# Optimization experiments

Measured on AMD Instinct MI355X. Metric: run time of the kernel, lower is better.

Reference implementation:

```python
import jax, jax.numpy as jnp
import numpy as np

B, T, F2, F1 = 64, 300, 2944, 1472
RED, H, K, LN = 256, 32, 15, 7          # reduced_size, hidden_size, att_frams, layer_num
CA_RED = 320
N_CROP = T - 2 * (K - 1)                # 272 frames after the two k=15 convs
PYR = [2 ** j for j in range(1, LN)]    # [2,4,8,16,32,64]


def _pool_matrix(N, sizes):
    """Stacked AdaptiveAvgPool1d matrices: rows average torch-style bins."""
    mats = []
    for m in sizes:
        P = np.zeros((m, N), np.float32)
        for i in range(m):
            s = (i * N) // m
            e = -((-(i + 1) * N) // m)  # ceil((i+1)*N/m)
            P[i, s:e] = 1.0 / (e - s)
        mats.append(P)
    return jnp.asarray(np.concatenate(mats, 0))  # [sum(sizes), N]


def setup_inputs() -> dict:
    key = jax.random.key(0)
    ks = jax.random.split(key, 24)
    g = lambda k, sh, s=0.05: (jax.random.normal(k, sh) * s).astype(jnp.float32)
    inp = {
        "input": jax.random.normal(ks[0], (B, T, F2), jnp.float32),
        "input_length": jnp.full((B,), T, jnp.int64),
        "mean_var": g(ks[1], (F1,), 1.0),
        "std_var": jax.random.uniform(ks[2], (F1,), jnp.float32, 0.5, 1.5),
        "mean_mean": g(ks[3], (F1,), 1.0),
        "std_mean": jax.random.uniform(ks[4], (F1,), jnp.float32, 0.5, 1.5),
        # ChannelAttention params
        "ca_fc1_w": g(ks[5], (CA_RED, F2)), "ca_fc1_b": g(ks[6], (CA_RED,)),
        "ca_fc2_w": g(ks[7], (F2, CA_RED)), "ca_fc2_b": g(ks[8], (F2,)),
        # ANN (n_ANNlayers=1 -> only fc0 used)
        "ann_w": g(ks[9], (RED, F1)), "ann_b": g(ks[10], (RED,)),
        # GRU (torch gate order r,z,n)
        "gru_w_ih": g(ks[11], (3 * H, RED)), "gru_w_hh": g(ks[12], (3 * H, H)),
        "gru_b_ih": g(ks[13], (3 * H,)), "gru_b_hh": g(ks[14], (3 * H,)),
        # frame-quality head
        "q_w": g(ks[15], (1, H)), "q_b": g(ks[16], (1,)),
        # temporal attention convs
        "att_w1": g(ks[17], (1, H, K)), "att_b1": g(ks[18], (1,)),
        "att_w2": g(ks[19], (1, 1, K)), "att_b2": g(ks[20], (1,)),
        "qreg2_w": g(ks[21], (1, 2 ** LN - 1)), "qreg2_b": g(ks[22], (1,)),
    }
    return inp


def _gru(x, w_ih, w_hh, b_ih, b_hh):
    xg = jnp.einsum("btf,gf->btg", x, w_ih) + b_ih  # [B,T,3H]

    def step(h, xt):
        hg = h @ w_hh.T + b_hh
        xr, xz, xn = jnp.split(xt, 3, -1)
        hr, hz, hn = jnp.split(hg, 3, -1)
        r = jax.nn.sigmoid(xr + hr)
        z = jax.nn.sigmoid(xz + hz)
        n = jnp.tanh(xn + r * hn)
        h = (1.0 - z) * n + z * h
        return h, h

    h0 = jnp.zeros((x.shape[0], H), x.dtype)
    _, hs = jax.lax.scan(step, h0, jnp.swapaxes(xg, 0, 1))
    return jnp.swapaxes(hs, 0, 1)  # [B,T,H]


def reference(input, input_length, mean_var, std_var, mean_mean, std_mean,
              ca_fc1_w, ca_fc1_b, ca_fc2_w, ca_fc2_b, ann_w, ann_b,
              gru_w_ih, gru_w_hh, gru_b_ih, gru_b_hh, q_w, q_b,
              att_w1, att_b1, att_w2, att_b2, qreg2_w, qreg2_b):
    # --- ChannelAttention: normalize var/mean halves, sigmoid gate, fuse to 1472-d
    x_var = (input[..., :F1] - mean_var) / std_var
    x_mean = (input[..., F1:] - mean_mean) / std_mean
    xn = jnp.concatenate([x_var, x_mean], -1)                      # [B,T,2944]
    w = jax.nn.sigmoid(jnp.maximum(xn @ ca_fc1_w.T + ca_fc1_b, 0.0) @ ca_fc2_w.T + ca_fc2_b)
    feat = w[..., :F1] * x_var + w[..., F1:] * x_mean              # [B,T,1472]

    # --- ANN (single layer) + GRU
    feat = feat @ ann_w.T + ann_b                                  # [B,T,256]
    outs = _gru(feat, gru_w_ih, gru_w_hh, gru_b_ih, gru_b_hh)      # [B,T,32]

    # --- temporal attention: Conv1d(H,1,15) -> ReLU -> Conv1d(1,1,15) -> tanh
    xc = jnp.swapaxes(outs, 1, 2)                                  # [B,H,T]
    dn = ("NCH", "OIH", "NCH")
    a = jax.lax.conv_general_dilated(xc, att_w1, (1,), "VALID", dimension_numbers=dn) + att_b1[None, :, None]
    a = jnp.maximum(a, 0.0)
    a = jax.lax.conv_general_dilated(a, att_w2, (1,), "VALID", dimension_numbers=dn) + att_b2[None, :, None]
    att = jnp.tanh(a[:, 0, :])                                     # [B,N_CROP]

    q_fet = att[..., None] * outs[:, K - 1: T - (K - 1), :]        # [B,N_CROP,H]

    # --- pyramid pooling: row0 = plain mean, rest = attention-weighted means
    P = _pool_matrix(N_CROP, PYR)                                  # [126, N_CROP]
    row0 = q_fet.mean(1, keepdims=True)                            # [B,1,H]
    num = jnp.einsum("mn,bnh->bmh", P, q_fet)                      # [B,126,H]
    den = jnp.einsum("mn,bn->bm", P, att)[..., None]               # [B,126,1]
    q_pool = jnp.concatenate([row0, num / den], 1)                 # [B,127,H]

    q_each = (q_pool @ q_w.T + q_b)[..., 0]                        # [B,127]
    score = q_each @ qreg2_w.T + qreg2_b                           # [B,1]
    return score
```

## Files before the change

kernel.cpp:

```cpp
#include <hip/hip_runtime.h>


typedef unsigned short u16t;
typedef unsigned int   u32t;
typedef float  f32x4 __attribute__((ext_vector_type(4)));
typedef u32t   u32x4 __attribute__((ext_vector_type(4)));
typedef __bf16 bf16x8 __attribute__((ext_vector_type(8)));

__device__ __forceinline__ f32x4 mfma_b(u32x4 a, u32x4 b, f32x4 c){
  return __builtin_amdgcn_mfma_f32_16x16x32_bf16(
      __builtin_bit_cast(bf16x8, a), __builtin_bit_cast(bf16x8, b), c, 0, 0, 0);
}

#define GLDS16(SRC, DST)                                                    \
  __builtin_amdgcn_global_load_lds(                                         \
      (const __attribute__((address_space(1))) void*)(SRC),                 \
      (__attribute__((address_space(3))) void*)(DST), 16, 0, 0)

__device__ __forceinline__ u32t resid(u32t u){
  float d = __uint_as_float(u) - __uint_as_float(u & 0xFFFF0000u);
  return __float_as_uint(d);
}

__device__ __forceinline__ void split8_3(u32x4 a, u32x4 b,
                                         u32x4& H, u32x4& M, u32x4& L){
  u32t r1[8], r2[8];
#pragma unroll
  for (int j = 0; j < 4; j++){ r1[j] = resid(a[j]); r1[4 + j] = resid(b[j]); }
#pragma unroll
  for (int j = 0; j < 8; j++){ r2[j] = resid(r1[j]); }
  H[0] = __builtin_amdgcn_perm(a[1], a[0], 0x07060302u);
  H[1] = __builtin_amdgcn_perm(a[3], a[2], 0x07060302u);
  H[2] = __builtin_amdgcn_perm(b[1], b[0], 0x07060302u);
  H[3] = __builtin_amdgcn_perm(b[3], b[2], 0x07060302u);
  M[0] = __builtin_amdgcn_perm(r1[1], r1[0], 0x07060302u);
  M[1] = __builtin_amdgcn_perm(r1[3], r1[2], 0x07060302u);
  M[2] = __builtin_amdgcn_perm(r1[5], r1[4], 0x07060302u);
  M[3] = __builtin_amdgcn_perm(r1[7], r1[6], 0x07060302u);
  L[0] = __builtin_amdgcn_perm(r2[1], r2[0], 0x07060302u);
  L[1] = __builtin_amdgcn_perm(r2[3], r2[2], 0x07060302u);
  L[2] = __builtin_amdgcn_perm(r2[5], r2[4], 0x07060302u);
  L[3] = __builtin_amdgcn_perm(r2[7], r2[6], 0x07060302u);
}

__device__ __forceinline__ void mfma6(const u32x4& AH, const u32x4& AM, const u32x4& AL,
                                      const u32x4& BH, const u32x4& BM, const u32x4& BL,
                                      f32x4& acc){
  acc = mfma_b(AL, BH, acc);
  acc = mfma_b(AM, BM, acc);
  acc = mfma_b(AH, BL, acc);
  acc = mfma_b(AM, BH, acc);
  acc = mfma_b(AH, BM, acc);
  acc = mfma_b(AH, BH, acc);
}

__global__ __launch_bounds__(256) void prep_params_kernel(
    const float* __restrict__ mv, const float* __restrict__ sv,
    const float* __restrict__ mm, const float* __restrict__ sm,
    double* __restrict__ mu, double* __restrict__ rinv){
  int f = blockIdx.x * 256 + threadIdx.x;
  if (f < 2944){
    if (f < 1472){ mu[f] = (double)mv[f]; rinv[f] = 1.0 / (double)sv[f]; }
    else         { mu[f] = (double)mm[f - 1472]; rinv[f] = 1.0 / (double)sm[f - 1472]; }
  }
}

__global__ __launch_bounds__(256) void fold_w1_kernel(
    const float* __restrict__ w, const double* __restrict__ rinv,
    float* __restrict__ w1p){
  int id = blockIdx.x * 256 + threadIdx.x;
  if (id < 320 * 2944)
    w1p[id] = (float)((double)w[id] * rinv[id % 2944]);
}

__global__ __launch_bounds__(64) void b1p_kernel(
    const float* __restrict__ w1, const float* __restrict__ b1,
    const double* __restrict__ mu, const double* __restrict__ rinv,
    float* __restrict__ b1p){
  int n = blockIdx.x, lane = threadIdx.x;
  double s = 0.0;
  for (int k = lane; k < 2944; k += 64)
    s += (double)w1[n * 2944 + k] * rinv[k] * mu[k];
#pragma unroll
  for (int o = 32; o > 0; o >>= 1) s += __shfl_xor(s, o);
  if (lane == 0) b1p[n] = (float)((double)b1[n] - s);
}

__global__ __launch_bounds__(256) void make_wc_kernel(
    const float* __restrict__ wih, const float* __restrict__ annw,
    const float* __restrict__ annb, const float* __restrict__ bih,
    float* __restrict__ wc, float* __restrict__ bc){
  int id = blockIdx.x * 256 + threadIdx.x;
  if (id < 96 * 1472){
    int g = id / 1472, k = id - g * 1472;
    double s = 0.0;
    for (int r = 0; r < 256; r++)
      s += (double)wih[g * 256 + r] * (double)annw[r * 1472 + k];
    wc[id] = (float)s;
  } else if (id < 96 * 1472 + 96){
    int g = id - 96 * 1472;
    double s = (double)bih[g];
    for (int r = 0; r < 256; r++)
      s += (double)wih[g * 256 + r] * (double)annb[r];
    bc[g] = (float)s;
  }
}

__global__ __launch_bounds__(256) void gemm1_kernel(
    const float* __restrict__ x, const float* __restrict__ w1p,
    const float* __restrict__ b1p, float* __restrict__ h1){
  __shared__ float lA[80 * 32];
  __shared__ float lB[320 * 32];
  const int tid = threadIdx.x, wave = tid >> 6, lane = tid & 63;
  const int m0 = blockIdx.x * 80;
  const int l8 = lane >> 3, l7 = lane & 7;
  f32x4 acc[5][5] = {};
  for (int k0 = 0; k0 < 2944; k0 += 32){
    __syncthreads();
    for (int i = wave; i < 10; i += 4){
      int row = i * 8 + l8;
      GLDS16(x + (size_t)(m0 + row) * 2944 + k0 + ((l7 ^ (row & 7)) << 2), lA + (i << 8));
    }
    for (int i = wave; i < 40; i += 4){
      int row = i * 8 + l8;
      GLDS16(w1p + (size_t)row * 2944 + k0 + ((l7 ^ (row & 7)) << 2), lB + (i << 8));
    }
    __syncthreads();
    const int g = lane >> 4, r15 = lane & 15;
    u32x4 AH[5], AM[5], AL[5];
#pragma unroll
    for (int fm = 0; fm < 5; fm++){
      int row = fm * 16 + r15;
      const char* base = (const char*)lA + (row << 7);
      u32x4 a0 = *(const u32x4*)(base + ((((g << 1) + 0) ^ (row & 7)) << 4));
      u32x4 a1 = *(const u32x4*)(base + ((((g << 1) + 1) ^ (row & 7)) << 4));
      split8_3(a0, a1, AH[fm], AM[fm], AL[fm]);
    }
#pragma unroll
    for (int fn = 0; fn < 5; fn++){
      int row = wave * 80 + fn * 16 + r15;
      const char* base = (const char*)lB + (row << 7);
      u32x4 b0 = *(const u32x4*)(base + ((((g << 1) + 0) ^ (row & 7)) << 4));
      u32x4 b1v = *(const u32x4*)(base + ((((g << 1) + 1) ^ (row & 7)) << 4));
      u32x4 BH, BM, BL; split8_3(b0, b1v, BH, BM, BL);
#pragma unroll
      for (int fm = 0; fm < 5; fm++)
        mfma6(AH[fm], AM[fm], AL[fm], BH, BM, BL, acc[fm][fn]);
    }
  }
#pragma unroll
  for (int fn = 0; fn < 5; fn++){
    int col = wave * 80 + fn * 16 + (lane & 15);
    float bias = b1p[col];
#pragma unroll
    for (int fm = 0; fm < 5; fm++){
      int mb = m0 + fm * 16 + ((lane >> 4) << 2);
#pragma unroll
      for (int r = 0; r < 4; r++)
        h1[(size_t)(mb + r) * 320 + col] = fmaxf(acc[fm][fn][r] + bias, 0.f);
    }
  }
}

__global__ __launch_bounds__(256) void gemm2_kernel(
    const float* __restrict__ h1, const float* __restrict__ w2,
    const float* __restrict__ b2, const float* __restrict__ x,
    const double* __restrict__ mu, const double* __restrict__ rinv,
    float* __restrict__ feat){
  __shared__ float lA[128 * 32];
  __shared__ float lB[128 * 32];
  const int tid = threadIdx.x, wave = tid >> 6, lane = tid & 63;
  const int wm = wave >> 1, wn = wave & 1;
  const int f0 = blockIdx.x * 64, m0 = blockIdx.y * 128;
  const int l8 = lane >> 3, l7 = lane & 7;
  f32x4 acc[4][4] = {};
  for (int k0 = 0; k0 < 320; k0 += 32){
    __syncthreads();
    for (int i = wave; i < 16; i += 4){
      int row = i * 8 + l8;
      GLDS16(h1 + (size_t)(m0 + row) * 320 + k0 + ((l7 ^ (row & 7)) << 2), lA + (i << 8));
    }
    for (int i = wave; i < 16; i += 4){
      int row = i * 8 + l8;
      int w2row = (((row >> 4) & 1) * 1472) + f0 + ((row >> 5) << 4) + (row & 15);
      GLDS16(w2 + (size_t)w2row * 320 + k0 + ((l7 ^ (row & 7)) << 2), lB + (i << 8));
    }
    __syncthreads();
    const int g = lane >> 4, r15 = lane & 15;
    u32x4 AH[4], AM[4], AL[4];
#pragma unroll
    for (int fm = 0; fm < 4; fm++){
      int row = wm * 64 + fm * 16 + r15;
      const char* base = (const char*)lA + (row << 7);
      u32x4 a0 = *(const u32x4*)(base + ((((g << 1) + 0) ^ (row & 7)) << 4));
      u32x4 a1 = *(const u32x4*)(base + ((((g << 1) + 1) ^ (row & 7)) << 4));
      split8_3(a0, a1, AH[fm], AM[fm], AL[fm]);
    }
#pragma unroll
    for (int fn = 0; fn < 4; fn++){
      int row = wn * 64 + fn * 16 + r15;
      const char* base = (const char*)lB + (row << 7);
      u32x4 b0 = *(const u32x4*)(base + ((((g << 1) + 0) ^ (row & 7)) << 4));
      u32x4 b1v = *(const u32x4*)(base + ((((g << 1) + 1) ^ (row & 7)) << 4));
      u32x4 BH, BM, BL; split8_3(b0, b1v, BH, BM, BL);
#pragma unroll
      for (int fm = 0; fm < 4; fm++)
        mfma6(AH[fm], AM[fm], AL[fm], BH, BM, BL, acc[fm][fn]);
    }
  }
#pragma unroll
  for (int cg = 0; cg < 2; cg++){
    int f = f0 + wn * 32 + cg * 16 + (lane & 15);
    float blo = b2[f], bhi = b2[1472 + f];
    double muv = mu[f], riv = rinv[f];
    double mum = mu[1472 + f], rim = rinv[1472 + f];
#pragma unroll
    for (int fm = 0; fm < 4; fm++){
      int mb = m0 + wm * 64 + fm * 16 + ((lane >> 4) << 2);
#pragma unroll
      for (int r = 0; r < 4; r++){
        int m = mb + r;
        float zl = acc[fm][2 * cg][r] + blo;
        float zh = acc[fm][2 * cg + 1][r] + bhi;
        float wl = 1.f / (1.f + expf(-zl));
        float wh = 1.f / (1.f + expf(-zh));
        float xv = (float)(((double)x[(size_t)m * 2944 + f] - muv) * riv);
        float xm = (float)(((double)x[(size_t)m * 2944 + 1472 + f] - mum) * rim);
        feat[(size_t)m * 1472 + f] = wl * xv + wh * xm;
      }
    }
  }
}

__global__ __launch_bounds__(256) void gemm3_kernel(
    const float* __restrict__ feat, const float* __restrict__ wc,
    const float* __restrict__ bc, float* __restrict__ xg){
  __shared__ float lA[64 * 64];
  __shared__ float lB[96 * 64];
  const int tid = threadIdx.x, wave = tid >> 6, lane = tid & 63;
  const int wm = wave >> 1, wn = wave & 1;
  const int m0 = blockIdx.x * 64;
  const int l4 = lane >> 4, l15 = lane & 15;
  f32x4 acc[2][3] = {};
  for (int k0 = 0; k0 < 1472; k0 += 64){
    __syncthreads();
    for (int i = wave; i < 16; i += 4){
      int row = i * 4 + l4;
      GLDS16(feat + (size_t)(m0 + row) * 1472 + k0 + ((l15 ^ (row & 15)) << 2), lA + (i << 8));
    }
    for (int i = wave; i < 24; i += 4){
      int row = i * 4 + l4;
      GLDS16(wc + (size_t)row * 1472 + k0 + ((l15 ^ (row & 15)) << 2), lB + (i << 8));
    }
    __syncthreads();
    const int g = lane >> 4, r15 = lane & 15;
#pragma unroll
    for (int ks = 0; ks < 2; ks++){
      u32x4 AH[2], AM[2], AL[2];
#pragma unroll
      for (int fm = 0; fm < 2; fm++){
        int row = wm * 32 + fm * 16 + r15;
        const char* base = (const char*)lA + (row << 8);
        u32x4 a0 = *(const u32x4*)(base + (((ks * 8 + 2 * g + 0) ^ (row & 15)) << 4));
        u32x4 a1 = *(const u32x4*)(base + (((ks * 8 + 2 * g + 1) ^ (row & 15)) << 4));
        split8_3(a0, a1, AH[fm], AM[fm], AL[fm]);
      }
#pragma unroll
      for (int fn = 0; fn < 3; fn++){
        int row = wn * 48 + fn * 16 + r15;
        const char* base = (const char*)lB + (row << 8);
        u32x4 b0 = *(const u32x4*)(base + (((ks * 8 + 2 * g + 0) ^ (row & 15)) << 4));
        u32x4 b1v = *(const u32x4*)(base + (((ks * 8 + 2 * g + 1) ^ (row & 15)) << 4));
        u32x4 BH, BM, BL; split8_3(b0, b1v, BH, BM, BL);
#pragma unroll
        for (int fm = 0; fm < 2; fm++)
          mfma6(AH[fm], AM[fm], AL[fm], BH, BM, BL, acc[fm][fn]);
      }
    }
  }
#pragma unroll
  for (int fn = 0; fn < 3; fn++){
    int col = wn * 48 + fn * 16 + (lane & 15);
    float bias = bc[col];
#pragma unroll
    for (int fm = 0; fm < 2; fm++){
      int mb = m0 + wm * 32 + fm * 16 + ((lane >> 4) << 2);
#pragma unroll
      for (int r = 0; r < 4; r++)
        xg[(size_t)(mb + r) * 96 + col] = acc[fm][fn][r] + bias;
    }
  }
}

__global__ __launch_bounds__(128) void gru_kernel(
    const float* __restrict__ xg, const float* __restrict__ whh,
    const float* __restrict__ bhh, float* __restrict__ outs){
  const int b = blockIdx.x, tid = threadIdx.x;
  __shared__ float hs[32];
  __shared__ double hg[96];
  double wr[32];
  double bias = 0.0;
  if (tid < 96){
#pragma unroll
    for (int j = 0; j < 32; j++) wr[j] = (double)whh[tid * 32 + j];
    bias = (double)bhh[tid];
  }
  if (tid < 32) hs[tid] = 0.f;
  __syncthreads();
  const float* xb = xg + (size_t)b * 300 * 96;
  float* ob = outs + (size_t)b * 300 * 32;
  for (int t = 0; t < 300; t++){
    if (tid < 96){
      double s0 = 0.0, s1 = 0.0;
#pragma unroll
      for (int j = 0; j < 16; j++){
        s0 += wr[j] * (double)hs[j];
        s1 += wr[16 + j] * (double)hs[16 + j];
      }
      hg[tid] = bias + s0 + s1;
    }
    __syncthreads();
    if (tid < 32){
      float xr  = xb[t * 96 + tid];
      float xz  = xb[t * 96 + 32 + tid];
      float xnv = xb[t * 96 + 64 + tid];
      float r = 1.f / (1.f + expf(-(float)((double)xr + hg[tid])));
      float z = 1.f / (1.f + expf(-(float)((double)xz + hg[32 + tid])));
      float n = tanhf((float)((double)xnv + (double)r * hg[64 + tid]));
      float h = (1.f - z) * n + z * hs[tid];
      hs[tid] = h;
      ob[t * 32 + tid] = h;
    }
    __syncthreads();
  }
}

__global__ __launch_bounds__(64) void attn_final_kernel(
    const float* __restrict__ outs, const float* __restrict__ w1,
    const float* __restrict__ b1, const float* __restrict__ w2,
    const float* __restrict__ b2, const float* __restrict__ qw,
    const float* __restrict__ qb, const float* __restrict__ rw,
    const float* __restrict__ rb, float* __restrict__ out){
  const int b = blockIdx.x, lane = threadIdx.x;
  __shared__ float a1[286];
  __shared__ double attv[272];
  __shared__ double sd[272];
  __shared__ float w1s[480];
  __shared__ float qws[32];
  const float* ob = outs + (size_t)b * 300 * 32;
  for (int i = lane; i < 480; i += 64) w1s[i] = w1[i];
  if (lane < 32) qws[lane] = qw[lane];
  __syncthreads();
  const double bb1 = (double)b1[0];
  for (int t = lane; t < 286; t += 64){
    double s = bb1;
    for (int k = 0; k < 15; k++){
      const float* row = ob + (t + k) * 32;
#pragma unroll
      for (int c = 0; c < 32; c++) s += (double)row[c] * (double)w1s[c * 15 + k];
    }
    a1[t] = fmaxf((float)s, 0.f);
  }
  __syncthreads();
  const double bb2 = (double)b2[0];
  for (int t = lane; t < 272; t += 64){
    double s = bb2;
#pragma unroll
    for (int k = 0; k < 15; k++) s += (double)a1[t + k] * (double)w2[k];
    double a = tanh(s);
    attv[t] = a;
    const float* row = ob + (t + 14) * 32;
    double d = 0.0;
#pragma unroll
    for (int c = 0; c < 32; c++) d += (double)row[c] * (double)qws[c];
    sd[t] = a * d;
  }
  __syncthreads();
  const double qb0 = (double)qb[0];
  double part = 0.0;
  double msum = 0.0;
  for (int t = lane; t < 272; t += 64) msum += sd[t];
  part += (double)rw[0] * (msum / 272.0);
  if (lane == 0) part += (double)rw[0] * qb0 + (double)rb[0];
  for (int j = lane; j < 126; j += 64){
    int mcur = 2, i = j;
    while (i >= mcur){ i -= mcur; mcur <<= 1; }
    int s = (i * 272) / mcur;
    int e = ((i + 1) * 272 + mcur - 1) / mcur;
    double S = 0.0, A = 0.0;
    for (int n = s; n < e; n++){ S += sd[n]; A += attv[n]; }
    part += (double)rw[1 + j] * (S / A + qb0);
  }
#pragma unroll
  for (int o = 32; o > 0; o >>= 1) part += __shfl_xor(part, o);
  if (lane == 0) out[b] = (float)part;
}

extern "C" void kernel_launch(void* const* d_in, const int* in_sizes, int n_in,
                              void* d_out, int out_size, void* d_ws, size_t ws_size,
                              hipStream_t stream){
  const float* input     = (const float*)d_in[0];
  const float* mean_var  = (const float*)d_in[2];
  const float* std_var   = (const float*)d_in[3];
  const float* mean_mean = (const float*)d_in[4];
  const float* std_mean  = (const float*)d_in[5];
  const float* ca1w = (const float*)d_in[6];
  const float* ca1b = (const float*)d_in[7];
  const float* ca2w = (const float*)d_in[8];
  const float* ca2b = (const float*)d_in[9];
  const float* annw = (const float*)d_in[10];
  const float* annb = (const float*)d_in[11];
  const float* wih  = (const float*)d_in[12];
  const float* whh  = (const float*)d_in[13];
  const float* bih  = (const float*)d_in[14];
  const float* bhh  = (const float*)d_in[15];
  const float* qw   = (const float*)d_in[16];
  const float* qb   = (const float*)d_in[17];
  const float* aw1  = (const float*)d_in[18];
  const float* ab1  = (const float*)d_in[19];
  const float* aw2  = (const float*)d_in[20];
  const float* ab2  = (const float*)d_in[21];
  const float* rw   = (const float*)d_in[22];
  const float* rb   = (const float*)d_in[23];
  float* out = (float*)d_out;

  char* ws = (char*)d_ws;
  size_t off = 0;
  auto alloc = [&](size_t bytes){
    size_t o = off; off += (bytes + 255) & ~(size_t)255; return o;
  };
  float* h1    = (float*)(ws + alloc((size_t)19200 * 320 * 4));
  float* feat  = (float*)(ws + alloc((size_t)19200 * 1472 * 4));
  float* xg    = (float*)(ws + alloc((size_t)19200 * 96 * 4));
  float* outsb = (float*)(ws + alloc((size_t)19200 * 32 * 4));
  float* w1p   = (float*)(ws + alloc((size_t)320 * 2944 * 4));
  float* wc    = (float*)(ws + alloc((size_t)96 * 1472 * 4));
  double* mu   = (double*)(ws + alloc(2944 * 8));
  double* rinv = (double*)(ws + alloc(2944 * 8));
  float* b1p   = (float*)(ws + alloc(320 * 4));
  float* bc    = (float*)(ws + alloc(96 * 4));
  (void)ws_size; (void)in_sizes; (void)n_in; (void)out_size;

  prep_params_kernel<<<12, 256, 0, stream>>>(mean_var, std_var, mean_mean, std_mean, mu, rinv);
  fold_w1_kernel<<<3680, 256, 0, stream>>>(ca1w, rinv, w1p);
  b1p_kernel<<<320, 64, 0, stream>>>(ca1w, ca1b, mu, rinv, b1p);
  make_wc_kernel<<<553, 256, 0, stream>>>(wih, annw, annb, bih, wc, bc);
  gemm1_kernel<<<240, 256, 0, stream>>>(input, w1p, b1p, h1);
  gemm2_kernel<<<dim3(23, 150), 256, 0, stream>>>(h1, ca2w, ca2b, input, mu, rinv, feat);
  gemm3_kernel<<<300, 256, 0, stream>>>(feat, wc, bc, xg);
  gru_kernel<<<64, 128, 0, stream>>>(xg, whh, bhh, outsb);
  attn_final_kernel<<<64, 64, 0, stream>>>(outsb, aw1, ab1, aw2, ab2, qw, qb, rw, rb, out);
}
```

Baseline: 924.9 us.

## Pre-split operands into bf16 hi/mid/lo planes to skip in-loop splitting

Weights and the intermediate activations h1 and feat are now stored as three bf16 planes (high, mid, low) written by the producing kernel. The GEMM inner loops load those planes straight into fragments instead of re-splitting fp32 data on every tile. gemm1 is also retiled to 64x160 blocks with a 2D grid, and the gemm2 grid order is swapped. This removes repeated split ALU work, for example the B split in gemm1 that was redone by every M-block. In exchange, intermediate traffic grows by 1.5x (three 16-bit planes versus one fp32) and there is an extra split kernel for w2.

Result: slower. 1.021 ms (+10.4%).

```diff
diff --git a/kernel.cpp b/kernel.cpp
--- a/kernel.cpp
+++ b/kernel.cpp
@@ -16,6 +16,16 @@
   __builtin_amdgcn_global_load_lds(                                         \
       (const __attribute__((address_space(1))) void*)(SRC),                 \
       (__attribute__((address_space(3))) void*)(DST), 16, 0, 0)
+
+__device__ __forceinline__ void split3(float x, u16t& h, u16t& m, u16t& l){
+  u32t u = __float_as_uint(x);
+  h = (u16t)(u >> 16);
+  float d1 = x - __uint_as_float(u & 0xFFFF0000u);
+  u32t u1 = __float_as_uint(d1);
+  m = (u16t)(u1 >> 16);
+  float d2 = d1 - __uint_as_float(u1 & 0xFFFF0000u);
+  l = (u16t)(__float_as_uint(d2) >> 16);
+}
 
 __device__ __forceinline__ u32t resid(u32t u){
   float d = __uint_as_float(u) - __uint_as_float(u & 0xFFFF0000u);
@@ -65,12 +75,21 @@
   }
 }
 
-__global__ __launch_bounds__(256) void fold_w1_kernel(
+__global__ __launch_bounds__(256) void split3_w1_kernel(
     const float* __restrict__ w, const double* __restrict__ rinv,
-    float* __restrict__ w1p){
+    u16t* __restrict__ wh, u16t* __restrict__ wm, u16t* __restrict__ wl){
   int id = blockIdx.x * 256 + threadIdx.x;
-  if (id < 320 * 2944)
-    w1p[id] = (float)((double)w[id] * rinv[id % 2944]);
+  if (id < 320 * 2944){
+    float v = (float)((double)w[id] * rinv[id % 2944]);
+    split3(v, wh[id], wm[id], wl[id]);
+  }
+}
+
+__global__ __launch_bounds__(256) void split3_plain_kernel(
+    const float* __restrict__ w, u16t* __restrict__ wh, u16t* __restrict__ wm,
+    u16t* __restrict__ wl, int n){
+  int id = blockIdx.x * 256 + threadIdx.x;
+  if (id < n) split3(w[id], wh[id], wm[id], wl[id]);
 }
 
 __global__ __launch_bounds__(64) void b1p_kernel(
@@ -89,14 +108,15 @@
 __global__ __launch_bounds__(256) void make_wc_kernel(
     const float* __restrict__ wih, const float* __restrict__ annw,
     const float* __restrict__ annb, const float* __restrict__ bih,
-    float* __restrict__ wc, float* __restrict__ bc){
+    u16t* __restrict__ wch, u16t* __restrict__ wcm, u16t* __restrict__ wcl,
+    float* __restrict__ bc){
   int id = blockIdx.x * 256 + threadIdx.x;
   if (id < 96 * 1472){
     int g = id / 1472, k = id - g * 1472;
     double s = 0.0;
     for (int r = 0; r < 256; r++)
       s += (double)wih[g * 256 + r] * (double)annw[r * 1472 + k];
-    wc[id] = (float)s;
+    split3((float)s, wch[id], wcm[id], wcl[id]);
   } else if (id < 96 * 1472 + 96){
     int g = id - 96 * 1472;
     double s = (double)bih[g];
@@ -107,30 +127,38 @@
 }
 
 __global__ __launch_bounds__(256) void gemm1_kernel(
-    const float* __restrict__ x, const float* __restrict__ w1p,
-    const float* __restrict__ b1p, float* __restrict__ h1){
-  __shared__ float lA[80 * 32];
-  __shared__ float lB[320 * 32];
+    const float* __restrict__ x,
+    const u16t* __restrict__ w1h, const u16t* __restrict__ w1m,
+    const u16t* __restrict__ w1l, const float* __restrict__ b1p,
+    u16t* __restrict__ h1h, u16t* __restrict__ h1m, u16t* __restrict__ h1l){
+  __shared__ float lA[64 * 32];
+  __shared__ u16t lBh[160 * 32], lBm[160 * 32], lBl[160 * 32];
   const int tid = threadIdx.x, wave = tid >> 6, lane = tid & 63;
-  const int m0 = blockIdx.x * 80;
-  const int l8 = lane >> 3, l7 = lane & 7;
-  f32x4 acc[5][5] = {};
+  const int wm = wave >> 1, wn = wave & 1;
+  const int m0 = blockIdx.y * 64, n0 = blockIdx.x * 160;
+  const int ar = lane >> 3, as = lane & 7;
+  const int br = lane >> 2, bs = lane & 3;
+  f32x4 acc[2][5] = {};
   for (int k0 = 0; k0 < 2944; k0 += 32){
     __syncthreads();
+#pragma unroll
+    for (int i = wave; i < 8; i += 4){
+      int row = i * 8 + ar;
+      GLDS16(x + (size_t)(m0 + row) * 2944 + k0 + ((as ^ (row & 7)) << 2), lA + (i << 8));
+    }
     for (int i = wave; i < 10; i += 4){
-      int row = i * 8 + l8;
-      GLDS16(x + (size_t)(m0 + row) * 2944 + k0 + ((l7 ^ (row & 7)) << 2), lA + (i << 8));
-    }
-    for (int i = wave; i < 40; i += 4){
-      int row = i * 8 + l8;
-      GLDS16(w1p + (size_t)row * 2944 + k0 + ((l7 ^ (row & 7)) << 2), lB + (i << 8));
+      int row = i * 16 + br;
+      size_t src = (size_t)(n0 + row) * 2944 + k0 + ((bs ^ ((row >> 1) & 3)) << 3);
+      GLDS16(w1h + src, lBh + (i << 9));
+      GLDS16(w1m + src, lBm + (i << 9));
+      GLDS16(w1l + src, lBl + (i << 9));
     }
     __syncthreads();
     const int g = lane >> 4, r15 = lane & 15;
-    u32x4 AH[5], AM[5], AL[5];
-#pragma unroll
-    for (int fm = 0; fm < 5; fm++){
-      int row = fm * 16 + r15;
+    u32x4 AH[2], AM[2], AL[2];
+#pragma unroll
+    for (int fm = 0; fm < 2; fm++){
+      int row = wm * 32 + fm * 16 + r15;
       const char* base = (const char*)lA + (row << 7);
       u32x4 a0 = *(const u32x4*)(base + ((((g << 1) + 0) ^ (row & 7)) << 4));
       u32x4 a1 = *(const u32x4*)(base + ((((g << 1) + 1) ^ (row & 7)) << 4));
@@ -138,52 +166,62 @@
     }
 #pragma unroll
     for (int fn = 0; fn < 5; fn++){
-      int row = wave * 80 + fn * 16 + r15;
-      const char* base = (const char*)lB + (row << 7);
-      u32x4 b0 = *(const u32x4*)(base + ((((g << 1) + 0) ^ (row & 7)) << 4));
-      u32x4 b1v = *(const u32x4*)(base + ((((g << 1) + 1) ^ (row & 7)) << 4));
-      u32x4 BH, BM, BL; split8_3(b0, b1v, BH, BM, BL);
-#pragma unroll
-      for (int fm = 0; fm < 5; fm++)
+      int row = wn * 80 + fn * 16 + r15;
+      int off = (row << 6) + ((g ^ ((row >> 1) & 3)) << 4);
+      u32x4 BH = *(const u32x4*)((const char*)lBh + off);
+      u32x4 BM = *(const u32x4*)((const char*)lBm + off);
+      u32x4 BL = *(const u32x4*)((const char*)lBl + off);
+#pragma unroll
+      for (int fm = 0; fm < 2; fm++)
         mfma6(AH[fm], AM[fm], AL[fm], BH, BM, BL, acc[fm][fn]);
     }
   }
 #pragma unroll
   for (int fn = 0; fn < 5; fn++){
-    int col = wave * 80 + fn * 16 + (lane & 15);
+    int col = n0 + wn * 80 + fn * 16 + (lane & 15);
     float bias = b1p[col];
 #pragma unroll
-    for (int fm = 0; fm < 5; fm++){
-      int mb = m0 + fm * 16 + ((lane >> 4) << 2);
-#pragma unroll
-      for (int r = 0; r < 4; r++)
-        h1[(size_t)(mb + r) * 320 + col] = fmaxf(acc[fm][fn][r] + bias, 0.f);
+    for (int fm = 0; fm < 2; fm++){
+      int mb = m0 + wm * 32 + fm * 16 + ((lane >> 4) << 2);
+#pragma unroll
+      for (int r = 0; r < 4; r++){
+        float v = fmaxf(acc[fm][fn][r] + bias, 0.f);
+        size_t o = (size_t)(mb + r) * 320 + col;
+        split3(v, h1h[o], h1m[o], h1l[o]);
+      }
     }
   }
 }
 
 __global__ __launch_bounds__(256) void gemm2_kernel(
-    const float* __restrict__ h1, const float* __restrict__ w2,
-    const float* __restrict__ b2, const float* __restrict__ x,
-    const double* __restrict__ mu, const double* __restrict__ rinv,
-    float* __restrict__ feat){
-  __shared__ float lA[128 * 32];
-  __shared__ float lB[128 * 32];
+    const u16t* __restrict__ h1h, const u16t* __restrict__ h1m,
+    const u16t* __restrict__ h1l,
+    const u16t* __restrict__ w2h, const u16t* __restrict__ w2m,
+    const u16t* __restrict__ w2l, const float* __restrict__ b2,
+    const float* __restrict__ x, const double* __restrict__ mu,
+    const double* __restrict__ rinv,
+    u16t* __restrict__ feath, u16t* __restrict__ featm, u16t* __restrict__ featl){
+  __shared__ u16t lAh[128 * 32], lAm[128 * 32], lAl[128 * 32];
+  __shared__ u16t lBh[128 * 32], lBm[128 * 32], lBl[128 * 32];
   const int tid = threadIdx.x, wave = tid >> 6, lane = tid & 63;
   const int wm = wave >> 1, wn = wave & 1;
-  const int f0 = blockIdx.x * 64, m0 = blockIdx.y * 128;
-  const int l8 = lane >> 3, l7 = lane & 7;
+  const int m0 = blockIdx.x * 128, f0 = blockIdx.y * 64;
+  const int br = lane >> 2, bs = lane & 3;
   f32x4 acc[4][4] = {};
   for (int k0 = 0; k0 < 320; k0 += 32){
     __syncthreads();
-    for (int i = wave; i < 16; i += 4){
-      int row = i * 8 + l8;
-      GLDS16(h1 + (size_t)(m0 + row) * 320 + k0 + ((l7 ^ (row & 7)) << 2), lA + (i << 8));
-    }
-    for (int i = wave; i < 16; i += 4){
-      int row = i * 8 + l8;
+    for (int i = wave; i < 8; i += 4){
+      int row = i * 16 + br;
+      int cs = (bs ^ ((row >> 1) & 3)) << 3;
+      size_t sa = (size_t)(m0 + row) * 320 + k0 + cs;
+      GLDS16(h1h + sa, lAh + (i << 9));
+      GLDS16(h1m + sa, lAm + (i << 9));
+      GLDS16(h1l + sa, lAl + (i << 9));
       int w2row = (((row >> 4) & 1) * 1472) + f0 + ((row >> 5) << 4) + (row & 15);
-      GLDS16(w2 + (size_t)w2row * 320 + k0 + ((l7 ^ (row & 7)) << 2), lB + (i << 8));
+      size_t sb = (size_t)w2row * 320 + k0 + cs;
+      GLDS16(w2h + sb, lBh + (i << 9));
+      GLDS16(w2m + sb, lBm + (i << 9));
+      GLDS16(w2l + sb, lBl + (i << 9));
     }
     __syncthreads();
     const int g = lane >> 4, r15 = lane & 15;
@@ -191,18 +229,18 @@
 #pragma unroll
     for (int fm = 0; fm < 4; fm++){
       int row = wm * 64 + fm * 16 + r15;
-      const char* base = (const char*)lA + (row << 7);
-      u32x4 a0 = *(const u32x4*)(base + ((((g << 1) + 0) ^ (row & 7)) << 4));
-      u32x4 a1 = *(const u32x4*)(base + ((((g << 1) + 1) ^ (row & 7)) << 4));
-      split8_3(a0, a1, AH[fm], AM[fm], AL[fm]);
+      int off = (row << 6) + ((g ^ ((row >> 1) & 3)) << 4);
+      AH[fm] = *(const u32x4*)((const char*)lAh + off);
+      AM[fm] = *(const u32x4*)((const char*)lAm + off);
+      AL[fm] = *(const u32x4*)((const char*)lAl + off);
     }
 #pragma unroll
     for (int fn = 0; fn < 4; fn++){
       int row = wn * 64 + fn * 16 + r15;
-      const char* base = (const char*)lB + (row << 7);
-      u32x4 b0 = *(const u32x4*)(base + ((((g << 1) + 0) ^ (row & 7)) << 4));
-      u32x4 b1v = *(const u32x4*)(base + ((((g << 1) + 1) ^ (row & 7)) << 4));
-      u32x4 BH, BM, BL; split8_3(b0, b1v, BH, BM, BL);
+      int off = (row << 6) + ((g ^ ((row >> 1) & 3)) << 4);
+      u32x4 BH = *(const u32x4*)((const char*)lBh + off);
+      u32x4 BM = *(const u32x4*)((const char*)lBm + off);
+      u32x4 BL = *(const u32x4*)((const char*)lBl + off);
 #pragma unroll
       for (int fm = 0; fm < 4; fm++)
         mfma6(AH[fm], AM[fm], AL[fm], BH, BM, BL, acc[fm][fn]);
@@ -226,56 +264,67 @@
         float wh = 1.f / (1.f + expf(-zh));
         float xv = (float)(((double)x[(size_t)m * 2944 + f] - muv) * riv);
         float xm = (float)(((double)x[(size_t)m * 2944 + 1472 + f] - mum) * rim);
-        feat[(size_t)m * 1472 + f] = wl * xv + wh * xm;
+        float fv = wl * xv + wh * xm;
+        size_t o = (size_t)m * 1472 + f;
+        split3(fv, feath[o], featm[o], featl[o]);
       }
     }
   }
 }
 
 __global__ __launch_bounds__(256) void gemm3_kernel(
-    const float* __restrict__ feat, const float* __restrict__ wc,
-    const float* __restrict__ bc, float* __restrict__ xg){
-  __shared__ float lA[64 * 64];
-  __shared__ float lB[96 * 64];
+    const u16t* __restrict__ feath, const u16t* __restrict__ featm,
+    const u16t* __restrict__ featl,
+    const u16t* __restrict__ wch, const u16t* __restrict__ wcm,
+    const u16t* __restrict__ wcl, const float* __restrict__ bc,
+    float* __restrict__ xg){
+  __shared__ u16t lAh[64 * 32], lAm[64 * 32], lAl[64 * 32];
+  __shared__ u16t lBh[96 * 32], lBm[96 * 32], lBl[96 * 32];
   const int tid = threadIdx.x, wave = tid >> 6, lane = tid & 63;
   const int wm = wave >> 1, wn = wave & 1;
   const int m0 = blockIdx.x * 64;
-  const int l4 = lane >> 4, l15 = lane & 15;
+  const int br = lane >> 2, bs = lane & 3;
   f32x4 acc[2][3] = {};
-  for (int k0 = 0; k0 < 1472; k0 += 64){
-    __syncthreads();
-    for (int i = wave; i < 16; i += 4){
-      int row = i * 4 + l4;
-      GLDS16(feat + (size_t)(m0 + row) * 1472 + k0 + ((l15 ^ (row & 15)) << 2), lA + (i << 8));
-    }
-    for (int i = wave; i < 24; i += 4){
-      int row = i * 4 + l4;
-      GLDS16(wc + (size_t)row * 1472 + k0 + ((l15 ^ (row & 15)) << 2), lB + (i << 8));
+  for (int k0 = 0; k0 < 1472; k0 += 32){
+    __syncthreads();
+#pragma unroll
+    for (int i = wave; i < 4; i += 4){
+      int row = i * 16 + br;
+      int cs = (bs ^ ((row >> 1) & 3)) << 3;
+      size_t sa = (size_t)(m0 + row) * 1472 + k0 + cs;
+      GLDS16(feath + sa, lAh + (i << 9));
+      GLDS16(featm + sa, lAm + (i << 9));
+      GLDS16(featl + sa, lAl + (i << 9));
+    }
+    for (int i = wave; i < 6; i += 4){
+      int row = i * 16 + br;
+      int cs = (bs ^ ((row >> 1) & 3)) << 3;
+      size_t sb = (size_t)row * 1472 + k0 + cs;
+      GLDS16(wch + sb, lBh + (i << 9));
+      GLDS16(wcm + sb, lBm + (i << 9));
+      GLDS16(wcl + sb, lBl + (i << 9));
     }
     __syncthreads();
     const int g = lane >> 4, r15 = lane & 15;
-#pragma unroll
-    for (int ks = 0; ks < 2; ks++){
-      u32x4 AH[2], AM[2], AL[2];
-#pragma unroll
-      for (int fm = 0; fm < 2; fm++){
-        int row = wm * 32 + fm * 16 + r15;
-        const char* base = (const char*)lA + (row << 8);
-        u32x4 a0 = *(const u32x4*)(base + (((ks * 8 + 2 * g + 0) ^ (row & 15)) << 4));
-        u32x4 a1 = *(const u32x4*)(base + (((ks * 8 + 2 * g + 1) ^ (row & 15)) << 4));
-        split8_3(a0, a1, AH[fm], AM[fm], AL[fm]);
-      }
-#pragma unroll
-      for (int fn = 0; fn < 3; fn++){
-        int row = wn * 48 + fn * 16 + r15;
-        const char* base = (const char*)lB + (row << 8);
-        u32x4 b0 = *(const u32x4*)(base + (((ks * 8 + 2 * g + 0) ^ (row & 15)) << 4));
-        u32x4 b1v = *(const u32x4*)(base + (((ks * 8 + 2 * g + 1) ^ (row & 15)) << 4));
-        u32x4 BH, BM, BL; split8_3(b0, b1v, BH, BM, BL);
-#pragma unroll
-        for (int fm = 0; fm < 2; fm++)
-          mfma6(AH[fm], AM[fm], AL[fm], BH, BM, BL, acc[fm][fn]);
-      }
+    u32x4 AH[2], AM[2], AL[2];
+#pragma unroll
+    for (int fm = 0; fm < 2; fm++){
+      int row = wm * 32 + fm * 16 + r15;
+      int off = (row << 6) + ((g ^ ((row >> 1) & 3)) << 4);
+      AH[fm] = *(const u32x4*)((const char*)lAh + off);
+      AM[fm] = *(const u32x4*)((const char*)lAm + off);
+      AL[fm] = *(const u32x4*)((const char*)lAl + off);
+    }
+#pragma unroll
+    for (int fn = 0; fn < 3; fn++){
+      int row = wn * 48 + fn * 16 + r15;
+      int off = (row << 6) + ((g ^ ((row >> 1) & 3)) << 4);
+      u32x4 BH = *(const u32x4*)((const char*)lBh + off);
+      u32x4 BM = *(const u32x4*)((const char*)lBm + off);
+      u32x4 BL = *(const u32x4*)((const char*)lBl + off);
+#pragma unroll
+      for (int fm = 0; fm < 2; fm++)
+        mfma6(AH[fm], AM[fm], AL[fm], BH, BM, BL, acc[fm][fn]);
     }
   }
 #pragma unroll
@@ -429,12 +478,24 @@
   auto alloc = [&](size_t bytes){
     size_t o = off; off += (bytes + 255) & ~(size_t)255; return o;
   };
-  float* h1    = (float*)(ws + alloc((size_t)19200 * 320 * 4));
-  float* feat  = (float*)(ws + alloc((size_t)19200 * 1472 * 4));
+  const size_t H1 = (size_t)19200 * 320, FT = (size_t)19200 * 1472;
+  u16t* h1h = (u16t*)(ws + alloc(H1 * 2));
+  u16t* h1m = (u16t*)(ws + alloc(H1 * 2));
+  u16t* h1l = (u16t*)(ws + alloc(H1 * 2));
+  u16t* feath = (u16t*)(ws + alloc(FT * 2));
+  u16t* featm = (u16t*)(ws + alloc(FT * 2));
+  u16t* featl = (u16t*)(ws + alloc(FT * 2));
   float* xg    = (float*)(ws + alloc((size_t)19200 * 96 * 4));
   float* outsb = (float*)(ws + alloc((size_t)19200 * 32 * 4));
-  float* w1p   = (float*)(ws + alloc((size_t)320 * 2944 * 4));
-  float* wc    = (float*)(ws + alloc((size_t)96 * 1472 * 4));
+  u16t* w1h = (u16t*)(ws + alloc((size_t)320 * 2944 * 2));
+  u16t* w1m = (u16t*)(ws + alloc((size_t)320 * 2944 * 2));
+  u16t* w1l = (u16t*)(ws + alloc((size_t)320 * 2944 * 2));
+  u16t* w2h = (u16t*)(ws + alloc((size_t)2944 * 320 * 2));
+  u16t* w2m = (u16t*)(ws + alloc((size_t)2944 * 320 * 2));
+  u16t* w2l = (u16t*)(ws + alloc((size_t)2944 * 320 * 2));
+  u16t* wch = (u16t*)(ws + alloc((size_t)96 * 1472 * 2));
+  u16t* wcm = (u16t*)(ws + alloc((size_t)96 * 1472 * 2));
+  u16t* wcl = (u16t*)(ws + alloc((size_t)96 * 1472 * 2));
   double* mu   = (double*)(ws + alloc(2944 * 8));
   double* rinv = (double*)(ws + alloc(2944 * 8));
   float* b1p   = (float*)(ws + alloc(320 * 4));
@@ -442,12 +503,14 @@
   (void)ws_size; (void)in_sizes; (void)n_in; (void)out_size;
 
   prep_params_kernel<<<12, 256, 0, stream>>>(mean_var, std_var, mean_mean, std_mean, mu, rinv);
-  fold_w1_kernel<<<3680, 256, 0, stream>>>(ca1w, rinv, w1p);
+  split3_w1_kernel<<<3680, 256, 0, stream>>>(ca1w, rinv, w1h, w1m, w1l);
+  split3_plain_kernel<<<3680, 256, 0, stream>>>(ca2w, w2h, w2m, w2l, 2944 * 320);
   b1p_kernel<<<320, 64, 0, stream>>>(ca1w, ca1b, mu, rinv, b1p);
-  make_wc_kernel<<<553, 256, 0, stream>>>(wih, annw, annb, bih, wc, bc);
-  gemm1_kernel<<<240, 256, 0, stream>>>(input, w1p, b1p, h1);
-  gemm2_kernel<<<dim3(23, 150), 256, 0, stream>>>(h1, ca2w, ca2b, input, mu, rinv, feat);
-  gemm3_kernel<<<300, 256, 0, stream>>>(feat, wc, bc, xg);
+  make_wc_kernel<<<553, 256, 0, stream>>>(wih, annw, annb, bih, wch, wcm, wcl, bc);
+  gemm1_kernel<<<dim3(2, 300), 256, 0, stream>>>(input, w1h, w1m, w1l, b1p, h1h, h1m, h1l);
+  gemm2_kernel<<<dim3(150, 23), 256, 0, stream>>>(h1h, h1m, h1l, w2h, w2m, w2l, ca2b,
+                                                  input, mu, rinv, feath, featm, featl);
+  gemm3_kernel<<<300, 256, 0, stream>>>(feath, featm, featl, wch, wcm, wcl, bc, xg);
   gru_kernel<<<64, 128, 0, stream>>>(xg, whh, bhh, outsb);
   attn_final_kernel<<<64, 64, 0, stream>>>(outsb, aw1, ab1, aw2, ab2, qw, qb, rw, rb, out);
 }
```
